# Optimization experiments

Measured on AMD Instinct MI355X. Metric: run time of the kernel, lower is better.

The kernel has to match this reference:

```python
import jax, jax.numpy as jnp
import numpy as np

N_NODES = 50000
N_EDGES = 1600000
N_FEAT = 50
HID = 20
OUT_DIM = 10
N_GRAPHS = 64


def _glorot(key, shape):
    fan_in, fan_out = shape[0], shape[1]
    lim = float(np.sqrt(6.0 / (fan_in + fan_out)))
    return jax.random.uniform(key, shape, jnp.float32, -lim, lim)


def setup_inputs() -> dict:
    key = jax.random.key(0)
    ks = jax.random.split(key, 16)
    x = jax.random.normal(ks[0], (N_NODES, N_FEAT), jnp.float32)
    edge_index = jax.random.randint(ks[1], (2, N_EDGES), 0, N_NODES, jnp.int32)
    batch = jnp.sort(jax.random.randint(ks[2], (N_NODES,), 0, N_GRAPHS, jnp.int32))
    inp = {"x": x, "edge_index": edge_index, "batch": batch}
    # GraphConv layer params: lin_rel (weight+bias, applied to aggregated msgs), lin_root (no bias)
    dims = [(N_FEAT, HID), (HID, HID), (HID, HID)]
    for i, (di, do) in enumerate(dims, start=1):
        inp[f"W_rel{i}"] = _glorot(ks[3 * i], (di, do))
        inp[f"W_root{i}"] = _glorot(ks[3 * i + 1], (di, do))
        inp[f"b{i}"] = jnp.zeros((do,), jnp.float32)
    # final Linear on cat([max_pool, mean_pool]) -> in_features = 2*HID
    inp["W_lin"] = _glorot(ks[13], (2 * HID, OUT_DIM))
    inp["b_lin"] = jnp.zeros((OUT_DIM,), jnp.float32)
    return inp


def _graph_conv(x, src, dst, W_rel, W_root, b):
    # PyG GraphConv: aggregate raw neighbor features (sum), then linear.
    agg = jax.ops.segment_sum(x[src], dst, num_segments=N_NODES)  # [N, d_in]
    return agg @ W_rel + x @ W_root + b


def reference(x, edge_index, batch,
              W_rel1, W_root1, b1,
              W_rel2, W_root2, b2,
              W_rel3, W_root3, b3,
              W_lin, b_lin):
    src, dst = edge_index[0], edge_index[1]
    h = jax.nn.relu(_graph_conv(x, src, dst, W_rel1, W_root1, b1))
    h = jax.nn.relu(_graph_conv(h, src, dst, W_rel2, W_root2, b2))
    h = jax.nn.relu(_graph_conv(h, src, dst, W_rel3, W_root3, b3))
    # global max / mean pool per graph
    maxP = jax.ops.segment_max(h, batch, num_segments=N_GRAPHS)  # [G, HID]
    sums = jax.ops.segment_sum(h, batch, num_segments=N_GRAPHS)
    cnt = jax.ops.segment_sum(jnp.ones((h.shape[0], 1), h.dtype), batch, num_segments=N_GRAPHS)
    meanP = sums / jnp.maximum(cnt, 1.0)
    return jnp.concatenate([maxP, meanP], axis=-1) @ W_lin + b_lin
```

## Files before the change

kernel.cpp:

```cpp
#include <hip/hip_runtime.h>

#define N_NODES  50000
#define N_EDGES  1600000
#define N_FEAT   50
#define HID      20
#define OUT_DIM  10
#define N_GRAPHS 64

#define NBUCK 196
#define BCAP  10240
#define EPB   6250
#define YSTR  32
#define GEMMB 977

__device__ __forceinline__ unsigned short f2bf(float f) {
    unsigned int u = __float_as_uint(f);
    u += 0x7FFFu + ((u >> 16) & 1u);
    return (unsigned short)(u >> 16);
}
__device__ __forceinline__ unsigned int pk2(float f0, float f1) {
    return (unsigned int)f2bf(f0) | ((unsigned int)f2bf(f1) << 16);
}
__device__ __forceinline__ float blo(unsigned int u) { return __uint_as_float(u << 16); }
__device__ __forceinline__ float bhi(unsigned int u) { return __uint_as_float(u & 0xFFFF0000u); }

__device__ __forceinline__ void addrow(const unsigned short* __restrict__ yb,
                                       int sn, float* a) {
    const unsigned short* p = yb + (size_t)sn * YSTR;
    uint4 q0 = *(const uint4*)(p);
    uint4 q1 = *(const uint4*)(p + 8);
    uint2 q2 = *(const uint2*)(p + 16);
    a[0] += blo(q0.x); a[1] += bhi(q0.x); a[2] += blo(q0.y); a[3] += bhi(q0.y);
    a[4] += blo(q0.z); a[5] += bhi(q0.z); a[6] += blo(q0.w); a[7] += bhi(q0.w);
    a[8] += blo(q1.x); a[9] += bhi(q1.x); a[10] += blo(q1.y); a[11] += bhi(q1.y);
    a[12] += blo(q1.z); a[13] += bhi(q1.z); a[14] += blo(q1.w); a[15] += bhi(q1.w);
    a[16] += blo(q2.x); a[17] += bhi(q2.x); a[18] += blo(q2.y); a[19] += bhi(q2.y);
}


__global__ __launch_bounds__(1024) void k1_scatter_gemm(
        const int* __restrict__ dst, const int* __restrict__ srcv,
        int* __restrict__ gcur, unsigned int* __restrict__ padded,
        const float* __restrict__ x, const float* __restrict__ Wrel,
        const float* __restrict__ Wroot, const float* __restrict__ bb,
        unsigned short* __restrict__ y, float* __restrict__ acc,
        float* __restrict__ gmax, float* __restrict__ gsum, float* __restrict__ gcnt) {
    __shared__ char smem[41728];
    int t = threadIdx.x;
    if (blockIdx.x < 256) {
        unsigned short* rnk = (unsigned short*)smem;
        unsigned int*   ep2 = (unsigned int*)(smem + 12544);
        int* cnt   = (int*)(smem + 37632);
        int* scn   = cnt + 256;
        int* lofs  = scn + 256;
        int* gbase = lofs + 256;
        if (blockIdx.x == 0) {
            for (int i = t; i < N_GRAPHS * HID; i += 1024) { gmax[i] = 0.f; gsum[i] = 0.f; }
            if (t < N_GRAPHS) gcnt[t] = 0.f;
        }
        if (t < 256) cnt[t] = 0;
        __syncthreads();
        int e0 = blockIdx.x * EPB;
        for (int i = t; i < EPB; i += 1024) {
            int d = dst[e0 + i];
            rnk[i] = (unsigned short)atomicAdd(&cnt[d >> 8], 1);
        }
        __syncthreads();
        if (t < 256) scn[t] = cnt[t];
        __syncthreads();
        for (int d = 1; d < 256; d <<= 1) {
            int u = 0;
            if (t < 256 && t >= d) u = scn[t - d];
            __syncthreads();
            if (t < 256) scn[t] += u;
            __syncthreads();
        }
        if (t < 256) lofs[t] = scn[t] - cnt[t];
        if (t < NBUCK) gbase[t] = t * BCAP + atomicAdd(&gcur[t], cnt[t]);
        __syncthreads();
        for (int i = t; i < EPB; i += 1024) {
            unsigned int d = (unsigned int)dst[e0 + i];
            unsigned int s = (unsigned int)srcv[e0 + i];
            ep2[lofs[d >> 8] + rnk[i]] = (d << 16) | s;
        }
        __syncthreads();
        for (int i = t; i < EPB; i += 1024) {
            unsigned int e = ep2[i];
            int bk = e >> 24;
            int gp = gbase[bk] + (i - lofs[bk]);
            if (gp < (bk + 1) * BCAP) padded[gp] = e;
        }
    } else {
        float* sWrel  = (float*)smem;
        float* sWroot = sWrel + N_FEAT * HID;
        for (int i = t; i < N_FEAT * HID; i += 1024) { sWrel[i] = Wrel[i]; sWroot[i] = Wroot[i]; }
        __syncthreads();
        int idx = (blockIdx.x - 256) * 1024 + t;
        if (idx < N_NODES * HID) {
            int n = idx / HID, j = idx % HID;
            const float* xr = x + n * N_FEAT;
            float a0 = 0.f, a1 = bb[j];
            #pragma unroll
            for (int k = 0; k < N_FEAT; ++k) {
                float xv = xr[k];
                a0 = fmaf(xv, sWrel[k * HID + j], a0);
                a1 = fmaf(xv, sWroot[k * HID + j], a1);
            }
            y[(size_t)n * YSTR + j] = f2bf(a0);
            acc[idx] = a1;
        }
    }
}


__global__ __launch_bounds__(1024) void k2_build_gather(
        const int* __restrict__ gcur, const unsigned int* __restrict__ padded,
        unsigned short* __restrict__ csr16, int* __restrict__ startg,
        int* __restrict__ cntg, unsigned short* __restrict__ permg,
        const unsigned short* __restrict__ y_in, const float* __restrict__ accp,
        const float* __restrict__ Wrel, const float* __restrict__ Wroot,
        const float* __restrict__ bb,
        unsigned short* __restrict__ y_out, float* __restrict__ acc_out) {
    __shared__ unsigned short eo[BCAP];
    __shared__ char uni[20480];
    __shared__ float sWrel[HID * HID], sWroot[HID * HID], sb[HID];
    __shared__ int cnt[256], scn[256], s_start[256], s_cnt[256];
    __shared__ unsigned short sperm[256];
    unsigned short* rnk = (unsigned short*)uni;
    float*          rh  = (float*)uni;
    int g = blockIdx.x, t = threadIdx.x;
    int base = g * BCAP;
    int m = min(gcur[g], BCAP);
    int n0 = g * 256;
    int nvalid = min(256, N_NODES - n0);
    for (int i = t; i < HID * HID; i += 1024) { sWrel[i] = Wrel[i]; sWroot[i] = Wroot[i]; }
    if (t < HID) sb[t] = bb[t];
    if (t < 256) cnt[t] = 0;
    __syncthreads();
    for (int i = t; i < m; i += 1024) {
        int local = (padded[base + i] >> 16) & 255;
        rnk[i] = (unsigned short)atomicAdd(&cnt[local], 1);
    }
    __syncthreads();
    if (t < 256) { s_cnt[t] = cnt[t]; scn[t] = cnt[t]; }
    __syncthreads();
    for (int d = 1; d < 256; d <<= 1) {
        int u = 0;
        if (t < 256 && t >= d) u = scn[t - d];
        __syncthreads();
        if (t < 256) scn[t] += u;
        __syncthreads();
    }
    if (t < 256) {
        s_start[t] = scn[t] - s_cnt[t];
        if (t < nvalid) { startg[n0 + t] = base + s_start[t]; cntg[n0 + t] = s_cnt[t]; }
    }
    __syncthreads();
    for (int i = t; i < m; i += 1024) {
        unsigned int e = padded[base + i];
        int local = (e >> 16) & 255;
        eo[s_start[local] + rnk[i]] = (unsigned short)(e & 0xFFFFu);
    }
    __syncthreads();
    for (int i = t; i < m; i += 1024) csr16[base + i] = eo[i];
    if (t < 256) {
        int d = s_cnt[t], rank = 0;
        for (int j2 = 0; j2 < 256; ++j2) {
            int dj = s_cnt[j2];
            rank += (dj > d) || (dj == d && j2 < t);
        }
        sperm[rank] = (unsigned short)t;
    }
    __syncthreads();
    if (t < 256) permg[g * 256 + t] = sperm[t];
    bool act = t < 512;
    int slot = t >> 1, half = t & 1;
    float a[HID];
    #pragma unroll
    for (int j = 0; j < HID; ++j) a[j] = 0.f;
    int nl = 0; bool ok = false; int a0 = 0, cn = 0;
    if (act) {
        nl = sperm[slot];
        ok = nl < nvalid;
        if (ok) { a0 = s_start[nl]; cn = s_cnt[nl]; }
    }
    if (ok) {
        #pragma unroll 2
        for (int k = half; k < cn; k += 2) addrow(y_in, eo[a0 + k], a);
        if (half == 0) {
            const float4* ar = (const float4*)(accp + (size_t)(n0 + nl) * HID);
            #pragma unroll
            for (int q = 0; q < 5; ++q) {
                float4 v = ar[q];
                a[q*4+0] += v.x; a[q*4+1] += v.y; a[q*4+2] += v.z; a[q*4+3] += v.w;
            }
        }
    }
    if (ok && half == 0) {
        #pragma unroll
        for (int q = 0; q < 5; ++q)
            *(float4*)&rh[nl * HID + q * 4] =
                make_float4(a[q*4], a[q*4+1], a[q*4+2], a[q*4+3]);
    }
    __syncthreads();
    if (ok && half == 1) {
        #pragma unroll
        for (int q = 0; q < 5; ++q) {
            float4 v = *(float4*)&rh[nl * HID + q * 4];
            v.x += a[q*4]; v.y += a[q*4+1]; v.z += a[q*4+2]; v.w += a[q*4+3];
            *(float4*)&rh[nl * HID + q * 4] = v;
        }
    }
    __syncthreads();
    for (int i = t; i < nvalid * 5; i += 1024) {
        int n = i / 5, j0 = (i % 5) * 4;
        float y0 = 0.f, y1 = 0.f, y2 = 0.f, y3 = 0.f;
        float c0 = sb[j0], c1 = sb[j0+1], c2 = sb[j0+2], c3 = sb[j0+3];
        #pragma unroll
        for (int k = 0; k < HID; ++k) {
            float h = fmaxf(rh[n * HID + k], 0.f);
            const float* wr = sWrel  + k * HID + j0;
            const float* wo = sWroot + k * HID + j0;
            y0 = fmaf(h, wr[0], y0); y1 = fmaf(h, wr[1], y1);
            y2 = fmaf(h, wr[2], y2); y3 = fmaf(h, wr[3], y3);
            c0 = fmaf(h, wo[0], c0); c1 = fmaf(h, wo[1], c1);
            c2 = fmaf(h, wo[2], c2); c3 = fmaf(h, wo[3], c3);
        }
        *(uint2*)(y_out + (size_t)(n0 + n) * YSTR + j0) = make_uint2(pk2(y0, y1), pk2(y2, y3));
        *(float4*)(acc_out + (size_t)(n0 + n) * HID + j0) = make_float4(c0, c1, c2, c3);
    }
}


__global__ __launch_bounds__(1024) void k3_gather_gemm(
        const int* __restrict__ startg, const int* __restrict__ cntg,
        const unsigned short* __restrict__ csr16, const unsigned short* __restrict__ permg,
        const unsigned short* __restrict__ y_in, const float* __restrict__ accp,
        const float* __restrict__ Wrel, const float* __restrict__ Wroot,
        const float* __restrict__ bb,
        unsigned short* __restrict__ y_out, float* __restrict__ acc_out) {
    __shared__ float rh[256 * HID];
    __shared__ float rh2[256 * HID];
    __shared__ float sWrel[HID * HID], sWroot[HID * HID], sb[HID];
    __shared__ unsigned short sperm[256];
    int g = blockIdx.x, t = threadIdx.x;
    int n0 = g * 256;
    int nvalid = min(256, N_NODES - n0);
    for (int i = t; i < HID * HID; i += 1024) { sWrel[i] = Wrel[i]; sWroot[i] = Wroot[i]; }
    if (t < HID) sb[t] = bb[t];
    if (t < 256) sperm[t] = permg[g * 256 + t];
    __syncthreads();
    int slot = t >> 2, q = t & 3;
    int nl = sperm[slot];
    bool ok = nl < nvalid;
    float a[HID];
    #pragma unroll
    for (int j = 0; j < HID; ++j) a[j] = 0.f;
    if (ok) {
        int node = n0 + nl;
        int a0 = startg[node], cn = cntg[node];
        #pragma unroll 2
        for (int k = q; k < cn; k += 4) addrow(y_in, csr16[a0 + k], a);
        if (q == 0) {
            const float4* ar = (const float4*)(accp + (size_t)node * HID);
            #pragma unroll
            for (int qq = 0; qq < 5; ++qq) {
                float4 v = ar[qq];
                a[qq*4+0] += v.x; a[qq*4+1] += v.y; a[qq*4+2] += v.z; a[qq*4+3] += v.w;
            }
        }
    }
    if (ok && (q == 0 || q == 2)) {
        float* dstp = (q == 0) ? rh : rh2;
        #pragma unroll
        for (int qq = 0; qq < 5; ++qq)
            *(float4*)&dstp[nl * HID + qq * 4] =
                make_float4(a[qq*4], a[qq*4+1], a[qq*4+2], a[qq*4+3]);
    }
    __syncthreads();
    if (ok && (q == 1 || q == 3)) {
        float* dstp = (q == 1) ? rh : rh2;
        #pragma unroll
        for (int qq = 0; qq < 5; ++qq) {
            float4 v = *(float4*)&dstp[nl * HID + qq * 4];
            v.x += a[qq*4]; v.y += a[qq*4+1]; v.z += a[qq*4+2]; v.w += a[qq*4+3];
            *(float4*)&dstp[nl * HID + qq * 4] = v;
        }
    }
    __syncthreads();
    for (int i = t; i < nvalid * 5; i += 1024) {
        int n = i / 5, j0 = (i % 5) * 4;
        float y0 = 0.f, y1 = 0.f, y2 = 0.f, y3 = 0.f;
        float c0 = sb[j0], c1 = sb[j0+1], c2 = sb[j0+2], c3 = sb[j0+3];
        #pragma unroll
        for (int k = 0; k < HID; ++k) {
            float h = fmaxf(rh[n * HID + k] + rh2[n * HID + k], 0.f);
            const float* wr = sWrel  + k * HID + j0;
            const float* wo = sWroot + k * HID + j0;
            y0 = fmaf(h, wr[0], y0); y1 = fmaf(h, wr[1], y1);
            y2 = fmaf(h, wr[2], y2); y3 = fmaf(h, wr[3], y3);
            c0 = fmaf(h, wo[0], c0); c1 = fmaf(h, wo[1], c1);
            c2 = fmaf(h, wo[2], c2); c3 = fmaf(h, wo[3], c3);
        }
        *(uint2*)(y_out + (size_t)(n0 + n) * YSTR + j0) = make_uint2(pk2(y0, y1), pk2(y2, y3));
        *(float4*)(acc_out + (size_t)(n0 + n) * HID + j0) = make_float4(c0, c1, c2, c3);
    }
}


__global__ __launch_bounds__(1024) void k4_gather_pool(
        const int* __restrict__ startg, const int* __restrict__ cntg,
        const unsigned short* __restrict__ csr16, const unsigned short* __restrict__ permg,
        const unsigned short* __restrict__ y_in, const float* __restrict__ accp,
        const int* __restrict__ batch,
        float* __restrict__ gmax, float* __restrict__ gsum, float* __restrict__ gcnt,
        int* __restrict__ done, const float* __restrict__ Wlin,
        const float* __restrict__ blin, float* __restrict__ out) {
    __shared__ float rh[256 * HID];
    __shared__ float rh2[256 * HID];
    __shared__ float redm[51 * HID], reds[51 * HID];
    __shared__ unsigned short sperm[256];
    __shared__ int sbatch[256];
    __shared__ int seglo[16], seghi[16];
    __shared__ int lastFlag;
    int g = blockIdx.x, t = threadIdx.x;
    int n0 = g * 256;
    int nvalid = min(256, N_NODES - n0);
    if (t < 256) sperm[t] = permg[g * 256 + t];
    if (t < nvalid) sbatch[t] = batch[n0 + t];
    __syncthreads();
    int slot = t >> 2, q = t & 3;
    int nl = sperm[slot];
    bool ok = nl < nvalid;
    float a[HID];
    #pragma unroll
    for (int j = 0; j < HID; ++j) a[j] = 0.f;
    if (ok) {
        int node = n0 + nl;
        int a0 = startg[node], cn = cntg[node];
        #pragma unroll 2
        for (int k = q; k < cn; k += 4) addrow(y_in, csr16[a0 + k], a);
        if (q == 0) {
            const float4* ar = (const float4*)(accp + (size_t)node * HID);
            #pragma unroll
            for (int qq = 0; qq < 5; ++qq) {
                float4 v = ar[qq];
                a[qq*4+0] += v.x; a[qq*4+1] += v.y; a[qq*4+2] += v.z; a[qq*4+3] += v.w;
            }
        }
    }
    if (ok && (q == 0 || q == 2)) {
        float* dstp = (q == 0) ? rh : rh2;
        #pragma unroll
        for (int qq = 0; qq < 5; ++qq)
            *(float4*)&dstp[nl * HID + qq * 4] =
                make_float4(a[qq*4], a[qq*4+1], a[qq*4+2], a[qq*4+3]);
    }
    __syncthreads();
    if (ok && (q == 1 || q == 3)) {
        float* dstp = (q == 1) ? rh : rh2;
        #pragma unroll
        for (int qq = 0; qq < 5; ++qq) {
            float4 v = *(float4*)&dstp[nl * HID + qq * 4];
            v.x += a[qq*4]; v.y += a[qq*4+1]; v.z += a[qq*4+2]; v.w += a[qq*4+3];
            *(float4*)&dstp[nl * HID + qq * 4] = v;
        }
    }
    __syncthreads();
    int g0 = sbatch[0];
    int span = sbatch[nvalid - 1] - g0 + 1;
    if (t < nvalid) {
        int bi = sbatch[t] - g0;
        if (bi < 16) {
            if (t == 0 || sbatch[t - 1] != sbatch[t]) seglo[bi] = t;
            if (t == nvalid - 1 || sbatch[t + 1] != sbatch[t]) seghi[bi] = t + 1;
        }
    }
    __syncthreads();
    if (span > 16) span = 16;
    for (int li = 0; li < span; ++li) {
        int lo = seglo[li], hi = seghi[li];
        int r = t / HID, j = t % HID;
        if (r < 51) {
            float mx = 0.f, sm = 0.f;
            for (int n = lo + r; n < hi; n += 51) {
                float v = fmaxf(rh[n * HID + j] + rh2[n * HID + j], 0.f);
                mx = fmaxf(mx, v); sm += v;
            }
            redm[r * HID + j] = mx; reds[r * HID + j] = sm;
        }
        __syncthreads();
        if (t < HID) {
            float mm = 0.f, ss = 0.f;
            #pragma unroll 17
            for (int r2 = 0; r2 < 51; ++r2) {
                mm = fmaxf(mm, redm[r2 * HID + t]);
                ss += reds[r2 * HID + t];
            }
            atomicMax((int*)&gmax[(g0 + li) * HID + t], __float_as_int(mm));
            atomicAdd(&gsum[(g0 + li) * HID + t], ss);
        }
        if (t == HID) atomicAdd(&gcnt[g0 + li], (float)(hi - lo));
        __syncthreads();
    }
    if (t == 0) {
        __threadfence();
        lastFlag = (atomicAdd(done, 1) == NBUCK - 1);
    }
    __syncthreads();
    if (!lastFlag) return;
    __threadfence();
    float* sW = redm;
    for (int i = t; i < 2 * HID * OUT_DIM; i += 1024) sW[i] = Wlin[i];
    __syncthreads();
    if (t < N_GRAPHS * OUT_DIM) {
        int gg = t / OUT_DIM, o = t % OUT_DIM;
        float c = fmaxf(gcnt[gg], 1.0f);
        float av = blin[o];
        #pragma unroll
        for (int j = 0; j < HID; ++j) {
            av = fmaf(gmax[gg * HID + j], sW[j * OUT_DIM + o], av);
            av = fmaf(gsum[gg * HID + j] / c, sW[(HID + j) * OUT_DIM + o], av);
        }
        out[t] = av;
    }
}

extern "C" void kernel_launch(void* const* d_in, const int* in_sizes, int n_in,
                              void* d_out, int out_size, void* d_ws, size_t ws_size,
                              hipStream_t stream) {
    const float* x      = (const float*)d_in[0];
    const int*   ei     = (const int*)  d_in[1];
    const int*   batch  = (const int*)  d_in[2];
    const float* Wrel1  = (const float*)d_in[3];
    const float* Wroot1 = (const float*)d_in[4];
    const float* b1     = (const float*)d_in[5];
    const float* Wrel2  = (const float*)d_in[6];
    const float* Wroot2 = (const float*)d_in[7];
    const float* b2     = (const float*)d_in[8];
    const float* Wrel3  = (const float*)d_in[9];
    const float* Wroot3 = (const float*)d_in[10];
    const float* b3     = (const float*)d_in[11];
    const float* Wlin   = (const float*)d_in[12];
    const float* blin   = (const float*)d_in[13];
    float* out = (float*)d_out;

    char* ws = (char*)d_ws;
    const size_t YB = (size_t)N_NODES * YSTR * 2;
    const size_t AB = (size_t)N_NODES * HID * 4;
    const size_t PB = (size_t)NBUCK * BCAP * 4;
    const size_t CB = (size_t)NBUCK * BCAP * 2;
    const size_t NP = (size_t)NBUCK * 256;
    unsigned short* yA     = (unsigned short*)(ws);
    unsigned short* yB     = (unsigned short*)(ws + YB);
    float*          accA   = (float*)(ws + 2 * YB);
    float*          accB   = (float*)(ws + 2 * YB + AB);
    unsigned int*   padded = (unsigned int*)(ws + 2 * YB + 2 * AB);
    unsigned short* csr16  = (unsigned short*)(ws + 2 * YB + 2 * AB + PB);
    int*            startg = (int*)(ws + 2 * YB + 2 * AB + PB + CB);
    int*            cntg   = startg + NP;
    unsigned short* permg  = (unsigned short*)(cntg + NP);
    int*            gcur   = (int*)((char*)permg + NP * 2);
    int*            done   = gcur + NBUCK;
    float*          gmax   = (float*)(done + 4);
    float*          gsum   = gmax + N_GRAPHS * HID;
    float*          gcnt   = gsum + N_GRAPHS * HID;

    const int* src = ei;
    const int* dst = ei + N_EDGES;

    hipMemsetAsync(gcur, 0, (NBUCK + 1) * sizeof(int), stream);
    k1_scatter_gemm<<<256 + GEMMB, 1024, 0, stream>>>(dst, src, gcur, padded,
                                                      x, Wrel1, Wroot1, b1, yA, accA,
                                                      gmax, gsum, gcnt);
    k2_build_gather<<<NBUCK, 1024, 0, stream>>>(gcur, padded, csr16, startg, cntg, permg,
                                                yA, accA, Wrel2, Wroot2, b2, yB, accB);
    k3_gather_gemm<<<NBUCK, 1024, 0, stream>>>(startg, cntg, csr16, permg,
                                               yB, accB, Wrel3, Wroot3, b3, yA, accA);
    k4_gather_pool<<<NBUCK, 1024, 0, stream>>>(startg, cntg, csr16, permg,
                                               yA, accA, batch, gmax, gsum, gcnt,
                                               done, Wlin, blin, out);
}
```

Before: 117.2 us.

## Rebalance node partitioning: 250 buckets of 200 nodes, 500 small blocks for gather layers

Node buckets shrink from 256 nodes to 200, with a multiply-shift key replacing d>>8, so there are 250 buckets instead of 196. Layers 3 and 4 now run 500 blocks of 512 threads over 100 nodes each and sort degrees locally, which removes the global permutation array. Layer 2 switches to 4 threads per node reading its CSR from shared memory. The goal is better occupancy and load balance across the MI355X CUs, at the cost of redoing the per-block rank sort and adding more blocks to the final atomic reduction.

```diff
diff --git a/kernel.cpp b/kernel.cpp
--- a/kernel.cpp
+++ b/kernel.cpp
@@ -7,11 +7,14 @@
 #define OUT_DIM  10
 #define N_GRAPHS 64
 
-#define NBUCK 196
-#define BCAP  10240
+#define NBUCK 250
+#define NPB   200
+#define BCAP  8192
 #define EPB   6250
 #define YSTR  32
 #define GEMMB 977
+#define NPB3  100
+#define NBLK3 500
 
 __device__ __forceinline__ unsigned short f2bf(float f) {
     unsigned int u = __float_as_uint(f);
@@ -23,7 +26,9 @@
 }
 __device__ __forceinline__ float blo(unsigned int u) { return __uint_as_float(u << 16); }
 __device__ __forceinline__ float bhi(unsigned int u) { return __uint_as_float(u & 0xFFFF0000u); }
-
+__device__ __forceinline__ int dkey(unsigned int d) {
+    return (int)(((unsigned long long)d * 167773ull) >> 25);
+}
 __device__ __forceinline__ void addrow(const unsigned short* __restrict__ yb,
                                        int sn, float* a) {
     const unsigned short* p = yb + (size_t)sn * YSTR;
@@ -62,15 +67,15 @@
         __syncthreads();
         int e0 = blockIdx.x * EPB;
         for (int i = t; i < EPB; i += 1024) {
-            int d = dst[e0 + i];
-            rnk[i] = (unsigned short)atomicAdd(&cnt[d >> 8], 1);
+            unsigned int d = (unsigned int)dst[e0 + i];
+            rnk[i] = (unsigned short)atomicAdd(&cnt[dkey(d)], 1);
         }
         __syncthreads();
         if (t < 256) scn[t] = cnt[t];
         __syncthreads();
-        for (int d = 1; d < 256; d <<= 1) {
+        for (int d2 = 1; d2 < 256; d2 <<= 1) {
             int u = 0;
-            if (t < 256 && t >= d) u = scn[t - d];
+            if (t < 256 && t >= d2) u = scn[t - d2];
             __syncthreads();
             if (t < 256) scn[t] += u;
             __syncthreads();
@@ -81,14 +86,14 @@
         for (int i = t; i < EPB; i += 1024) {
             unsigned int d = (unsigned int)dst[e0 + i];
             unsigned int s = (unsigned int)srcv[e0 + i];
-            ep2[lofs[d >> 8] + rnk[i]] = (d << 16) | s;
+            ep2[lofs[dkey(d)] + rnk[i]] = (d << 16) | s;
         }
         __syncthreads();
         for (int i = t; i < EPB; i += 1024) {
             unsigned int e = ep2[i];
-            int bk = e >> 24;
-            int gp = gbase[bk] + (i - lofs[bk]);
-            if (gp < (bk + 1) * BCAP) padded[gp] = e;
+            int key = dkey(e >> 16);
+            int gp = gbase[key] + (i - lofs[key]);
+            if (gp < (key + 1) * BCAP) padded[gp] = e;
         }
     } else {
         float* sWrel  = (float*)smem;
@@ -116,179 +121,103 @@
 __global__ __launch_bounds__(1024) void k2_build_gather(
         const int* __restrict__ gcur, const unsigned int* __restrict__ padded,
         unsigned short* __restrict__ csr16, int* __restrict__ startg,
-        int* __restrict__ cntg, unsigned short* __restrict__ permg,
+        int* __restrict__ cntg,
         const unsigned short* __restrict__ y_in, const float* __restrict__ accp,
         const float* __restrict__ Wrel, const float* __restrict__ Wroot,
         const float* __restrict__ bb,
         unsigned short* __restrict__ y_out, float* __restrict__ acc_out) {
     __shared__ unsigned short eo[BCAP];
-    __shared__ char uni[20480];
+    __shared__ char uni[16384];
+    __shared__ float rh2[NPB * HID];
     __shared__ float sWrel[HID * HID], sWroot[HID * HID], sb[HID];
-    __shared__ int cnt[256], scn[256], s_start[256], s_cnt[256];
+    __shared__ int cnt[256], scn[256], sstart[256], scnt[256];
     __shared__ unsigned short sperm[256];
     unsigned short* rnk = (unsigned short*)uni;
     float*          rh  = (float*)uni;
     int g = blockIdx.x, t = threadIdx.x;
     int base = g * BCAP;
     int m = min(gcur[g], BCAP);
-    int n0 = g * 256;
-    int nvalid = min(256, N_NODES - n0);
+    int n0 = g * NPB;
     for (int i = t; i < HID * HID; i += 1024) { sWrel[i] = Wrel[i]; sWroot[i] = Wroot[i]; }
     if (t < HID) sb[t] = bb[t];
     if (t < 256) cnt[t] = 0;
     __syncthreads();
     for (int i = t; i < m; i += 1024) {
-        int local = (padded[base + i] >> 16) & 255;
+        int local = (int)(padded[base + i] >> 16) - n0;
         rnk[i] = (unsigned short)atomicAdd(&cnt[local], 1);
     }
     __syncthreads();
-    if (t < 256) { s_cnt[t] = cnt[t]; scn[t] = cnt[t]; }
-    __syncthreads();
-    for (int d = 1; d < 256; d <<= 1) {
+    if (t < 256) scn[t] = cnt[t];
+    __syncthreads();
+    for (int d2 = 1; d2 < 256; d2 <<= 1) {
         int u = 0;
-        if (t < 256 && t >= d) u = scn[t - d];
+        if (t < 256 && t >= d2) u = scn[t - d2];
         __syncthreads();
         if (t < 256) scn[t] += u;
         __syncthreads();
     }
     if (t < 256) {
-        s_start[t] = scn[t] - s_cnt[t];
-        if (t < nvalid) { startg[n0 + t] = base + s_start[t]; cntg[n0 + t] = s_cnt[t]; }
+        sstart[t] = scn[t] - cnt[t];
+        scnt[t] = cnt[t];
+        if (t < NPB) { startg[n0 + t] = base + sstart[t]; cntg[n0 + t] = cnt[t]; }
     }
     __syncthreads();
     for (int i = t; i < m; i += 1024) {
         unsigned int e = padded[base + i];
-        int local = (e >> 16) & 255;
-        eo[s_start[local] + rnk[i]] = (unsigned short)(e & 0xFFFFu);
+        int local = (int)(e >> 16) - n0;
+        eo[sstart[local] + rnk[i]] = (unsigned short)(e & 0xFFFFu);
     }
     __syncthreads();
     for (int i = t; i < m; i += 1024) csr16[base + i] = eo[i];
     if (t < 256) {
-        int d = s_cnt[t], rank = 0;
+        int d = scnt[t], rank = 0;
         for (int j2 = 0; j2 < 256; ++j2) {
-            int dj = s_cnt[j2];
+            int dj = scnt[j2];
             rank += (dj > d) || (dj == d && j2 < t);
         }
         sperm[rank] = (unsigned short)t;
     }
     __syncthreads();
-    if (t < 256) permg[g * 256 + t] = sperm[t];
-    bool act = t < 512;
-    int slot = t >> 1, half = t & 1;
-    float a[HID];
-    #pragma unroll
-    for (int j = 0; j < HID; ++j) a[j] = 0.f;
-    int nl = 0; bool ok = false; int a0 = 0, cn = 0;
-    if (act) {
-        nl = sperm[slot];
-        ok = nl < nvalid;
-        if (ok) { a0 = s_start[nl]; cn = s_cnt[nl]; }
-    }
-    if (ok) {
-        #pragma unroll 2
-        for (int k = half; k < cn; k += 2) addrow(y_in, eo[a0 + k], a);
-        if (half == 0) {
-            const float4* ar = (const float4*)(accp + (size_t)(n0 + nl) * HID);
-            #pragma unroll
-            for (int q = 0; q < 5; ++q) {
-                float4 v = ar[q];
-                a[q*4+0] += v.x; a[q*4+1] += v.y; a[q*4+2] += v.z; a[q*4+3] += v.w;
-            }
-        }
-    }
-    if (ok && half == 0) {
+    {
+        int slot = t >> 2, q = t & 3;
+        int nl = sperm[slot];
+        bool ok = nl < NPB;
+        float a[HID];
         #pragma unroll
-        for (int q = 0; q < 5; ++q)
-            *(float4*)&rh[nl * HID + q * 4] =
-                make_float4(a[q*4], a[q*4+1], a[q*4+2], a[q*4+3]);
-    }
-    __syncthreads();
-    if (ok && half == 1) {
-        #pragma unroll
-        for (int q = 0; q < 5; ++q) {
-            float4 v = *(float4*)&rh[nl * HID + q * 4];
-            v.x += a[q*4]; v.y += a[q*4+1]; v.z += a[q*4+2]; v.w += a[q*4+3];
-            *(float4*)&rh[nl * HID + q * 4] = v;
-        }
-    }
-    __syncthreads();
-    for (int i = t; i < nvalid * 5; i += 1024) {
-        int n = i / 5, j0 = (i % 5) * 4;
-        float y0 = 0.f, y1 = 0.f, y2 = 0.f, y3 = 0.f;
-        float c0 = sb[j0], c1 = sb[j0+1], c2 = sb[j0+2], c3 = sb[j0+3];
-        #pragma unroll
-        for (int k = 0; k < HID; ++k) {
-            float h = fmaxf(rh[n * HID + k], 0.f);
-            const float* wr = sWrel  + k * HID + j0;
-            const float* wo = sWroot + k * HID + j0;
-            y0 = fmaf(h, wr[0], y0); y1 = fmaf(h, wr[1], y1);
-            y2 = fmaf(h, wr[2], y2); y3 = fmaf(h, wr[3], y3);
-            c0 = fmaf(h, wo[0], c0); c1 = fmaf(h, wo[1], c1);
-            c2 = fmaf(h, wo[2], c2); c3 = fmaf(h, wo[3], c3);
-        }
-        *(uint2*)(y_out + (size_t)(n0 + n) * YSTR + j0) = make_uint2(pk2(y0, y1), pk2(y2, y3));
-        *(float4*)(acc_out + (size_t)(n0 + n) * HID + j0) = make_float4(c0, c1, c2, c3);
-    }
-}
-
-
-__global__ __launch_bounds__(1024) void k3_gather_gemm(
-        const int* __restrict__ startg, const int* __restrict__ cntg,
-        const unsigned short* __restrict__ csr16, const unsigned short* __restrict__ permg,
-        const unsigned short* __restrict__ y_in, const float* __restrict__ accp,
-        const float* __restrict__ Wrel, const float* __restrict__ Wroot,
-        const float* __restrict__ bb,
-        unsigned short* __restrict__ y_out, float* __restrict__ acc_out) {
-    __shared__ float rh[256 * HID];
-    __shared__ float rh2[256 * HID];
-    __shared__ float sWrel[HID * HID], sWroot[HID * HID], sb[HID];
-    __shared__ unsigned short sperm[256];
-    int g = blockIdx.x, t = threadIdx.x;
-    int n0 = g * 256;
-    int nvalid = min(256, N_NODES - n0);
-    for (int i = t; i < HID * HID; i += 1024) { sWrel[i] = Wrel[i]; sWroot[i] = Wroot[i]; }
-    if (t < HID) sb[t] = bb[t];
-    if (t < 256) sperm[t] = permg[g * 256 + t];
-    __syncthreads();
-    int slot = t >> 2, q = t & 3;
-    int nl = sperm[slot];
-    bool ok = nl < nvalid;
-    float a[HID];
-    #pragma unroll
-    for (int j = 0; j < HID; ++j) a[j] = 0.f;
-    if (ok) {
-        int node = n0 + nl;
-        int a0 = startg[node], cn = cntg[node];
-        #pragma unroll 2
-        for (int k = q; k < cn; k += 4) addrow(y_in, csr16[a0 + k], a);
-        if (q == 0) {
-            const float4* ar = (const float4*)(accp + (size_t)node * HID);
+        for (int j = 0; j < HID; ++j) a[j] = 0.f;
+        if (ok) {
+            int cb = sstart[nl], ce = cb + scnt[nl];
+            #pragma unroll 2
+            for (int k = cb + q; k < ce; k += 4) addrow(y_in, eo[k], a);
+            if (q == 0) {
+                const float4* ar = (const float4*)(accp + (size_t)(n0 + nl) * HID);
+                #pragma unroll
+                for (int qq = 0; qq < 5; ++qq) {
+                    float4 v = ar[qq];
+                    a[qq*4+0] += v.x; a[qq*4+1] += v.y; a[qq*4+2] += v.z; a[qq*4+3] += v.w;
+                }
+            }
+        }
+        if (ok && (q == 0 || q == 2)) {
+            float* dstp = (q == 0) ? rh : rh2;
+            #pragma unroll
+            for (int qq = 0; qq < 5; ++qq)
+                *(float4*)&dstp[nl * HID + qq * 4] =
+                    make_float4(a[qq*4], a[qq*4+1], a[qq*4+2], a[qq*4+3]);
+        }
+        __syncthreads();
+        if (ok && (q == 1 || q == 3)) {
+            float* dstp = (q == 1) ? rh : rh2;
             #pragma unroll
             for (int qq = 0; qq < 5; ++qq) {
-                float4 v = ar[qq];
-                a[qq*4+0] += v.x; a[qq*4+1] += v.y; a[qq*4+2] += v.z; a[qq*4+3] += v.w;
-            }
-        }
-    }
-    if (ok && (q == 0 || q == 2)) {
-        float* dstp = (q == 0) ? rh : rh2;
-        #pragma unroll
-        for (int qq = 0; qq < 5; ++qq)
-            *(float4*)&dstp[nl * HID + qq * 4] =
-                make_float4(a[qq*4], a[qq*4+1], a[qq*4+2], a[qq*4+3]);
-    }
-    __syncthreads();
-    if (ok && (q == 1 || q == 3)) {
-        float* dstp = (q == 1) ? rh : rh2;
-        #pragma unroll
-        for (int qq = 0; qq < 5; ++qq) {
-            float4 v = *(float4*)&dstp[nl * HID + qq * 4];
-            v.x += a[qq*4]; v.y += a[qq*4+1]; v.z += a[qq*4+2]; v.w += a[qq*4+3];
-            *(float4*)&dstp[nl * HID + qq * 4] = v;
-        }
-    }
-    __syncthreads();
-    for (int i = t; i < nvalid * 5; i += 1024) {
+                float4 v = *(float4*)&dstp[nl * HID + qq * 4];
+                v.x += a[qq*4]; v.y += a[qq*4+1]; v.z += a[qq*4+2]; v.w += a[qq*4+3];
+                *(float4*)&dstp[nl * HID + qq * 4] = v;
+            }
+        }
+        __syncthreads();
+    }
+    for (int i = t; i < NPB * 5; i += 1024) {
         int n = i / 5, j0 = (i % 5) * 4;
         float y0 = 0.f, y1 = 0.f, y2 = 0.f, y3 = 0.f;
         float c0 = sb[j0], c1 = sb[j0+1], c2 = sb[j0+2], c3 = sb[j0+3];
@@ -308,72 +237,174 @@
 }
 
 
-__global__ __launch_bounds__(1024) void k4_gather_pool(
+__global__ __launch_bounds__(512) void k3_gather_gemm(
         const int* __restrict__ startg, const int* __restrict__ cntg,
-        const unsigned short* __restrict__ csr16, const unsigned short* __restrict__ permg,
+        const unsigned short* __restrict__ csr16,
+        const unsigned short* __restrict__ y_in, const float* __restrict__ accp,
+        const float* __restrict__ Wrel, const float* __restrict__ Wroot,
+        const float* __restrict__ bb,
+        unsigned short* __restrict__ y_out, float* __restrict__ acc_out) {
+    __shared__ float rh[NPB3 * HID];
+    __shared__ float rh2[NPB3 * HID];
+    __shared__ float sWrel[HID * HID], sWroot[HID * HID], sb[HID];
+    __shared__ int sstart[128], scnt[128];
+    __shared__ unsigned short sperm[128];
+    int g = blockIdx.x, t = threadIdx.x;
+    int n0 = g * NPB3;
+    for (int i = t; i < HID * HID; i += 512) { sWrel[i] = Wrel[i]; sWroot[i] = Wroot[i]; }
+    if (t < HID) sb[t] = bb[t];
+    if (t < 128) {
+        scnt[t]   = (t < NPB3) ? cntg[n0 + t] : -1;
+        sstart[t] = (t < NPB3) ? startg[n0 + t] : 0;
+    }
+    __syncthreads();
+    if (t < 128) {
+        int d = scnt[t], rank = 0;
+        for (int j2 = 0; j2 < 128; ++j2) {
+            int dj = scnt[j2];
+            rank += (dj > d) || (dj == d && j2 < t);
+        }
+        sperm[rank] = (unsigned short)t;
+    }
+    __syncthreads();
+    {
+        int slot = t >> 2, q = t & 3;
+        int nl = sperm[slot];
+        bool ok = nl < NPB3;
+        float a[HID];
+        #pragma unroll
+        for (int j = 0; j < HID; ++j) a[j] = 0.f;
+        if (ok) {
+            int cb = sstart[nl], ce = cb + scnt[nl];
+            #pragma unroll 2
+            for (int k = cb + q; k < ce; k += 4) addrow(y_in, csr16[k], a);
+            if (q == 0) {
+                const float4* ar = (const float4*)(accp + (size_t)(n0 + nl) * HID);
+                #pragma unroll
+                for (int qq = 0; qq < 5; ++qq) {
+                    float4 v = ar[qq];
+                    a[qq*4+0] += v.x; a[qq*4+1] += v.y; a[qq*4+2] += v.z; a[qq*4+3] += v.w;
+                }
+            }
+        }
+        if (ok && (q == 0 || q == 2)) {
+            float* dstp = (q == 0) ? rh : rh2;
+            #pragma unroll
+            for (int qq = 0; qq < 5; ++qq)
+                *(float4*)&dstp[nl * HID + qq * 4] =
+                    make_float4(a[qq*4], a[qq*4+1], a[qq*4+2], a[qq*4+3]);
+        }
+        __syncthreads();
+        if (ok && (q == 1 || q == 3)) {
+            float* dstp = (q == 1) ? rh : rh2;
+            #pragma unroll
+            for (int qq = 0; qq < 5; ++qq) {
+                float4 v = *(float4*)&dstp[nl * HID + qq * 4];
+                v.x += a[qq*4]; v.y += a[qq*4+1]; v.z += a[qq*4+2]; v.w += a[qq*4+3];
+                *(float4*)&dstp[nl * HID + qq * 4] = v;
+            }
+        }
+        __syncthreads();
+    }
+    for (int i = t; i < NPB3 * 5; i += 512) {
+        int n = i / 5, j0 = (i % 5) * 4;
+        float y0 = 0.f, y1 = 0.f, y2 = 0.f, y3 = 0.f;
+        float c0 = sb[j0], c1 = sb[j0+1], c2 = sb[j0+2], c3 = sb[j0+3];
+        #pragma unroll
+        for (int k = 0; k < HID; ++k) {
+            float h = fmaxf(rh[n * HID + k] + rh2[n * HID + k], 0.f);
+            const float* wr = sWrel  + k * HID + j0;
+            const float* wo = sWroot + k * HID + j0;
+            y0 = fmaf(h, wr[0], y0); y1 = fmaf(h, wr[1], y1);
+            y2 = fmaf(h, wr[2], y2); y3 = fmaf(h, wr[3], y3);
+            c0 = fmaf(h, wo[0], c0); c1 = fmaf(h, wo[1], c1);
+            c2 = fmaf(h, wo[2], c2); c3 = fmaf(h, wo[3], c3);
+        }
+        *(uint2*)(y_out + (size_t)(n0 + n) * YSTR + j0) = make_uint2(pk2(y0, y1), pk2(y2, y3));
+        *(float4*)(acc_out + (size_t)(n0 + n) * HID + j0) = make_float4(c0, c1, c2, c3);
+    }
+}
+
+
+__global__ __launch_bounds__(512) void k4_gather_pool(
+        const int* __restrict__ startg, const int* __restrict__ cntg,
+        const unsigned short* __restrict__ csr16,
         const unsigned short* __restrict__ y_in, const float* __restrict__ accp,
         const int* __restrict__ batch,
         float* __restrict__ gmax, float* __restrict__ gsum, float* __restrict__ gcnt,
         int* __restrict__ done, const float* __restrict__ Wlin,
         const float* __restrict__ blin, float* __restrict__ out) {
-    __shared__ float rh[256 * HID];
-    __shared__ float rh2[256 * HID];
-    __shared__ float redm[51 * HID], reds[51 * HID];
-    __shared__ unsigned short sperm[256];
-    __shared__ int sbatch[256];
+    __shared__ float rh[NPB3 * HID];
+    __shared__ float rh2[NPB3 * HID];
+    __shared__ float redm[26 * HID], reds[26 * HID];
+    __shared__ int sstart[128], scnt[128];
+    __shared__ unsigned short sperm[128];
+    __shared__ int sbatch[NPB3];
     __shared__ int seglo[16], seghi[16];
     __shared__ int lastFlag;
     int g = blockIdx.x, t = threadIdx.x;
-    int n0 = g * 256;
-    int nvalid = min(256, N_NODES - n0);
-    if (t < 256) sperm[t] = permg[g * 256 + t];
-    if (t < nvalid) sbatch[t] = batch[n0 + t];
-    __syncthreads();
-    int slot = t >> 2, q = t & 3;
-    int nl = sperm[slot];
-    bool ok = nl < nvalid;
-    float a[HID];
-    #pragma unroll
-    for (int j = 0; j < HID; ++j) a[j] = 0.f;
-    if (ok) {
-        int node = n0 + nl;
-        int a0 = startg[node], cn = cntg[node];
-        #pragma unroll 2
-        for (int k = q; k < cn; k += 4) addrow(y_in, csr16[a0 + k], a);
-        if (q == 0) {
-            const float4* ar = (const float4*)(accp + (size_t)node * HID);
+    int n0 = g * NPB3;
+    if (t < 128) {
+        scnt[t]   = (t < NPB3) ? cntg[n0 + t] : -1;
+        sstart[t] = (t < NPB3) ? startg[n0 + t] : 0;
+    }
+    if (t < NPB3) sbatch[t] = batch[n0 + t];
+    __syncthreads();
+    if (t < 128) {
+        int d = scnt[t], rank = 0;
+        for (int j2 = 0; j2 < 128; ++j2) {
+            int dj = scnt[j2];
+            rank += (dj > d) || (dj == d && j2 < t);
+        }
+        sperm[rank] = (unsigned short)t;
+    }
+    __syncthreads();
+    {
+        int slot = t >> 2, q = t & 3;
+        int nl = sperm[slot];
+        bool ok = nl < NPB3;
+        float a[HID];
+        #pragma unroll
+        for (int j = 0; j < HID; ++j) a[j] = 0.f;
+        if (ok) {
+            int cb = sstart[nl], ce = cb + scnt[nl];
+            #pragma unroll 2
+            for (int k = cb + q; k < ce; k += 4) addrow(y_in, csr16[k], a);
+            if (q == 0) {
+                const float4* ar = (const float4*)(accp + (size_t)(n0 + nl) * HID);
+                #pragma unroll
+                for (int qq = 0; qq < 5; ++qq) {
+                    float4 v = ar[qq];
+                    a[qq*4+0] += v.x; a[qq*4+1] += v.y; a[qq*4+2] += v.z; a[qq*4+3] += v.w;
+                }
+            }
+        }
+        if (ok && (q == 0 || q == 2)) {
+            float* dstp = (q == 0) ? rh : rh2;
+            #pragma unroll
+            for (int qq = 0; qq < 5; ++qq)
+                *(float4*)&dstp[nl * HID + qq * 4] =
+                    make_float4(a[qq*4], a[qq*4+1], a[qq*4+2], a[qq*4+3]);
+        }
+        __syncthreads();
+        if (ok && (q == 1 || q == 3)) {
+            float* dstp = (q == 1) ? rh : rh2;
             #pragma unroll
             for (int qq = 0; qq < 5; ++qq) {
-                float4 v = ar[qq];
-                a[qq*4+0] += v.x; a[qq*4+1] += v.y; a[qq*4+2] += v.z; a[qq*4+3] += v.w;
-            }
-        }
-    }
-    if (ok && (q == 0 || q == 2)) {
-        float* dstp = (q == 0) ? rh : rh2;
-        #pragma unroll
-        for (int qq = 0; qq < 5; ++qq)
-            *(float4*)&dstp[nl * HID + qq * 4] =
-                make_float4(a[qq*4], a[qq*4+1], a[qq*4+2], a[qq*4+3]);
-    }
-    __syncthreads();
-    if (ok && (q == 1 || q == 3)) {
-        float* dstp = (q == 1) ? rh : rh2;
-        #pragma unroll
-        for (int qq = 0; qq < 5; ++qq) {
-            float4 v = *(float4*)&dstp[nl * HID + qq * 4];
-            v.x += a[qq*4]; v.y += a[qq*4+1]; v.z += a[qq*4+2]; v.w += a[qq*4+3];
-            *(float4*)&dstp[nl * HID + qq * 4] = v;
-        }
-    }
-    __syncthreads();
+                float4 v = *(float4*)&dstp[nl * HID + qq * 4];
+                v.x += a[qq*4]; v.y += a[qq*4+1]; v.z += a[qq*4+2]; v.w += a[qq*4+3];
+                *(float4*)&dstp[nl * HID + qq * 4] = v;
+            }
+        }
+        __syncthreads();
+    }
     int g0 = sbatch[0];
-    int span = sbatch[nvalid - 1] - g0 + 1;
-    if (t < nvalid) {
+    int span = sbatch[NPB3 - 1] - g0 + 1;
+    if (t < NPB3) {
         int bi = sbatch[t] - g0;
         if (bi < 16) {
             if (t == 0 || sbatch[t - 1] != sbatch[t]) seglo[bi] = t;
-            if (t == nvalid - 1 || sbatch[t + 1] != sbatch[t]) seghi[bi] = t + 1;
+            if (t == NPB3 - 1 || sbatch[t + 1] != sbatch[t]) seghi[bi] = t + 1;
         }
     }
     __syncthreads();
@@ -381,9 +412,9 @@
     for (int li = 0; li < span; ++li) {
         int lo = seglo[li], hi = seghi[li];
         int r = t / HID, j = t % HID;
-        if (r < 51) {
+        if (r < 25) {
             float mx = 0.f, sm = 0.f;
-            for (int n = lo + r; n < hi; n += 51) {
+            for (int n = lo + r; n < hi; n += 25) {
                 float v = fmaxf(rh[n * HID + j] + rh2[n * HID + j], 0.f);
                 mx = fmaxf(mx, v); sm += v;
             }
@@ -392,8 +423,8 @@
         __syncthreads();
         if (t < HID) {
             float mm = 0.f, ss = 0.f;
-            #pragma unroll 17
-            for (int r2 = 0; r2 < 51; ++r2) {
+            #pragma unroll
+            for (int r2 = 0; r2 < 25; ++r2) {
                 mm = fmaxf(mm, redm[r2 * HID + t]);
                 ss += reds[r2 * HID + t];
             }
@@ -405,16 +436,16 @@
     }
     if (t == 0) {
         __threadfence();
-        lastFlag = (atomicAdd(done, 1) == NBUCK - 1);
+        lastFlag = (atomicAdd(done, 1) == NBLK3 - 1);
     }
     __syncthreads();
     if (!lastFlag) return;
     __threadfence();
     float* sW = redm;
-    for (int i = t; i < 2 * HID * OUT_DIM; i += 1024) sW[i] = Wlin[i];
-    __syncthreads();
-    if (t < N_GRAPHS * OUT_DIM) {
-        int gg = t / OUT_DIM, o = t % OUT_DIM;
+    for (int i = t; i < 2 * HID * OUT_DIM; i += 512) sW[i] = Wlin[i];
+    __syncthreads();
+    for (int idx = t; idx < N_GRAPHS * OUT_DIM; idx += 512) {
+        int gg = idx / OUT_DIM, o = idx % OUT_DIM;
         float c = fmaxf(gcnt[gg], 1.0f);
         float av = blin[o];
         #pragma unroll
@@ -422,7 +453,7 @@
             av = fmaf(gmax[gg * HID + j], sW[j * OUT_DIM + o], av);
             av = fmaf(gsum[gg * HID + j] / c, sW[(HID + j) * OUT_DIM + o], av);
         }
-        out[t] = av;
+        out[idx] = av;
     }
 }
 
@@ -450,7 +481,6 @@
     const size_t AB = (size_t)N_NODES * HID * 4;
     const size_t PB = (size_t)NBUCK * BCAP * 4;
     const size_t CB = (size_t)NBUCK * BCAP * 2;
-    const size_t NP = (size_t)NBUCK * 256;
     unsigned short* yA     = (unsigned short*)(ws);
     unsigned short* yB     = (unsigned short*)(ws + YB);
     float*          accA   = (float*)(ws + 2 * YB);
@@ -458,9 +488,8 @@
     unsigned int*   padded = (unsigned int*)(ws + 2 * YB + 2 * AB);
     unsigned short* csr16  = (unsigned short*)(ws + 2 * YB + 2 * AB + PB);
     int*            startg = (int*)(ws + 2 * YB + 2 * AB + PB + CB);
-    int*            cntg   = startg + NP;
-    unsigned short* permg  = (unsigned short*)(cntg + NP);
-    int*            gcur   = (int*)((char*)permg + NP * 2);
+    int*            cntg   = startg + N_NODES;
+    int*            gcur   = cntg + N_NODES;
     int*            done   = gcur + NBUCK;
     float*          gmax   = (float*)(done + 4);
     float*          gsum   = gmax + N_GRAPHS * HID;
@@ -469,15 +498,15 @@
     const int* src = ei;
     const int* dst = ei + N_EDGES;
 
-    hipMemsetAsync(gcur, 0, (NBUCK + 1) * sizeof(int), stream);
+    hipMemsetAsync(gcur, 0, (NBUCK + 4) * sizeof(int), stream);
     k1_scatter_gemm<<<256 + GEMMB, 1024, 0, stream>>>(dst, src, gcur, padded,
                                                       x, Wrel1, Wroot1, b1, yA, accA,
                                                       gmax, gsum, gcnt);
-    k2_build_gather<<<NBUCK, 1024, 0, stream>>>(gcur, padded, csr16, startg, cntg, permg,
+    k2_build_gather<<<NBUCK, 1024, 0, stream>>>(gcur, padded, csr16, startg, cntg,
                                                 yA, accA, Wrel2, Wroot2, b2, yB, accB);
-    k3_gather_gemm<<<NBUCK, 1024, 0, stream>>>(startg, cntg, csr16, permg,
-                                               yB, accB, Wrel3, Wroot3, b3, yA, accA);
-    k4_gather_pool<<<NBUCK, 1024, 0, stream>>>(startg, cntg, csr16, permg,
-                                               yA, accA, batch, gmax, gsum, gcnt,
-                                               done, Wlin, blin, out);
-}
+    k3_gather_gemm<<<NBLK3, 512, 0, stream>>>(startg, cntg, csr16,
+                                              yB, accB, Wrel3, Wroot3, b3, yA, accA);
+    k4_gather_pool<<<NBLK3, 512, 0, stream>>>(startg, cntg, csr16,
+                                              yA, accA, batch, gmax, gsum, gcnt,
+                                              done, Wlin, blin, out);
+}
```

After: 127.6 us. +8.8%, slower.
